# Kernel tuning notes

Hardware: AMD Instinct MI355X
Metric: run time of the kernel (lower is better)

Reference implementation:

```python
import jax, jax.numpy as jnp
import numpy as np

N_NODES = 100000
N_EDGES = 1600000
IN_DIM = 128
N_HID = 128


def setup_inputs() -> dict:
    key = jax.random.key(0)
    k1, k2, k3, k4 = jax.random.split(key, 4)
    node_feature = jax.random.normal(k1, (N_NODES, IN_DIM), dtype=jnp.float32)
    edge_index = jax.random.randint(k2, (2, N_EDGES), 0, N_NODES, dtype=jnp.int64)
    # GCN layer weights (glorot-ish scale)
    W1 = jax.random.normal(k3, (IN_DIM, N_HID), dtype=jnp.float32) / np.sqrt(IN_DIM)
    b1 = jnp.zeros((N_HID,), dtype=jnp.float32)
    W2 = jax.random.normal(k4, (N_HID, N_HID), dtype=jnp.float32) / np.sqrt(N_HID)
    b2 = jnp.zeros((N_HID,), dtype=jnp.float32)
    return {"node_feature": node_feature, "edge_index": edge_index,
            "W1": W1, "b1": b1, "W2": W2, "b2": b2}


def _gcn_layer(x, W, b, row, col, n_nodes):
    """GCNConv: x' = D^-1/2 (A + I) D^-1/2 (x W) + b, symmetric norm with self-loops."""
    xt = x @ W  # [N, out]
    ones = jnp.ones(row.shape[0], dtype=xt.dtype)
    deg = jnp.zeros((n_nodes,), dtype=xt.dtype).at[col].add(ones) + 1.0  # +1 self-loop
    dinv = jax.lax.rsqrt(deg)  # [N]
    norm = dinv[row] * dinv[col]  # [E]
    # gather messages from source (row), scatter-add into destination (col)
    agg = jnp.zeros_like(xt).at[col].add(xt[row] * norm[:, None])
    agg = agg + xt * (dinv * dinv)[:, None]  # self-loop contribution
    return agg + b


def reference(node_feature, edge_index, W1, b1, W2, b2):
    row, col = edge_index[0], edge_index[1]
    n = node_feature.shape[0]
    h = _gcn_layer(node_feature, W1, b1, row, col, n)
    # F.dropout with training=False is identity (eval-mode reference)
    h = _gcn_layer(h, W2, b2, row, col, n)
    return h
```

## Files before the change

### kernel.cpp

```cpp
#include <hip/hip_runtime.h>

typedef unsigned short ushort_t;
typedef __attribute__((ext_vector_type(8))) short short8;
typedef __attribute__((ext_vector_type(8))) unsigned short us8v;
typedef __attribute__((ext_vector_type(4))) float f32x4;

__device__ __forceinline__ float b2f(unsigned short u) {
    union { unsigned int i; float f; } v; v.i = ((unsigned int)u) << 16; return v.f;
}
__device__ __forceinline__ unsigned short f2b(float f) {
    union { float f; unsigned int i; } v; v.f = f;
    unsigned int r = (v.i + 0x7FFF + ((v.i >> 16) & 1)) >> 16;
    return (unsigned short)r;
}

__device__ __forceinline__ void load_edge(const int* __restrict__ ei, int e, int E,
                                          int is64, int& s, int& d) {
    if (is64) {
        const long long* el = (const long long*)ei;
        s = (int)el[e]; d = (int)el[E + e];
    } else {
        s = ei[e]; d = ei[E + e];
    }
}

__device__ __forceinline__ int detect64(const int* __restrict__ ei, int t) {
    int z = 0;
    for (int i = t; i < 512; i += 256) z |= ei[2 * i + 1];
    return (__syncthreads_or(z) == 0);
}

__global__ void k_hist(const int* __restrict__ ei, int E, unsigned N,
                       int* __restrict__ bhist, int BSH, int NB) {
    __shared__ int lh[256];
    int t = threadIdx.x;
    for (int b = t; b < NB; b += 256) lh[b] = 0;
    int is64 = detect64(ei, t);
    int e0 = blockIdx.x * 4096;
    #pragma unroll
    for (int i = 0; i < 16; ++i) {
        int e = e0 + i * 256 + t;
        if (e < E) {
            int s, d; load_edge(ei, e, E, is64, s, d);
            if ((unsigned)s < N && (unsigned)d < N) atomicAdd(&lh[d >> BSH], 1);
        }
    }
    __syncthreads();
    for (int b = t; b < NB; b += 256) { int v = lh[b]; if (v) atomicAdd(&bhist[b], v); }
}

__global__ void k_scanb(const int* __restrict__ bhist, int NB,
                        int* __restrict__ bkbase, int* __restrict__ bkcur) {
    __shared__ int sd[256];
    int t = threadIdx.x;
    int v0 = (t < NB) ? bhist[t] : 0;
    sd[t] = v0;
    for (int o = 1; o < 256; o <<= 1) {
        __syncthreads();
        int v = (t >= o) ? sd[t - o] : 0;
        __syncthreads();
        sd[t] += v;
    }
    __syncthreads();
    if (t < NB) { int ex = sd[t] - v0; bkbase[t] = ex; bkcur[t] = ex; }
}

__global__ __launch_bounds__(256) void k_bucket(const int* __restrict__ ei, int E, unsigned N,
                                                int* __restrict__ bkcur,
                                                int* __restrict__ bs, int* __restrict__ bd,
                                                int BSH, int NB) {
    __shared__ int lss[4096];
    __shared__ int ldd[4096];
    __shared__ int lhist[256];
    __shared__ int lcur[256];
    int t = threadIdx.x;
    int e0 = blockIdx.x * 4096;
    for (int b = t; b < NB; b += 256) lhist[b] = 0;
    int is64 = detect64(ei, t);
    #pragma unroll
    for (int i = 0; i < 16; ++i) {
        int idx = i * 256 + t, e = e0 + idx;
        int s = -1, d = -1;
        if (e < E) {
            load_edge(ei, e, E, is64, s, d);
            if (!((unsigned)s < N && (unsigned)d < N)) d = -1;
        }
        lss[idx] = s; ldd[idx] = d;
        if (d >= 0) atomicAdd(&lhist[d >> BSH], 1);
    }
    __syncthreads();
    for (int b = t; b < NB; b += 256) {
        int v = lhist[b];
        lcur[b] = v ? atomicAdd(&bkcur[b], v) : 0;
    }
    __syncthreads();
    #pragma unroll
    for (int i = 0; i < 16; ++i) {
        int idx = i * 256 + t;
        int d = ldd[idx];
        if (d >= 0) {
            int p = atomicAdd(&lcur[d >> BSH], 1);
            bs[p] = lss[idx]; bd[p] = d;
        }
    }
}

__global__ void k_count2(const int* __restrict__ bd, const int* __restrict__ bkbase,
                         const int* __restrict__ bkcur, int N, int BSH,
                         int* __restrict__ cnt) {
    __shared__ int lc[512];
    int b = blockIdx.x, t = threadIdx.x;
    int nbase = b << BSH;
    int nn = min(1 << BSH, N - nbase);
    for (int j = t; j < nn; j += 256) lc[j] = 0;
    __syncthreads();
    int s0 = bkbase[b], s1 = bkcur[b];
    for (int i = s0 + t; i < s1; i += 256) atomicAdd(&lc[bd[i] - nbase], 1);
    __syncthreads();
    for (int j = t; j < nn; j += 256) cnt[nbase + j] = lc[j];
}

__global__ void k_assign(int* __restrict__ cnt, int N,
                         int* __restrict__ pos, float* __restrict__ dinv,
                         int* __restrict__ cursor, int* __restrict__ srcs,
                         int padidx) {
    __shared__ int sd[256];
    __shared__ int sbase;
    int t = threadIdx.x;
    int n = blockIdx.x * 256 + t;
    int c = (n < N) ? cnt[n] : 0;
    int cp = (c + 7) & ~7;
    sd[t] = cp;
    for (int o = 1; o < 256; o <<= 1) {
        __syncthreads();
        int v = (t >= o) ? sd[t - o] : 0;
        __syncthreads();
        sd[t] += v;
    }
    __syncthreads();
    if (t == 255) sbase = atomicAdd(cursor, sd[255]);
    __syncthreads();
    if (n < N) {
        int st = sbase + sd[t] - cp;
        pos[n] = st;
        dinv[n] = rsqrtf((float)c + 1.0f);
        cnt[n] = cp;
        for (int q = c; q < cp; ++q) srcs[st + q] = padidx;
    }
}

__global__ void k_fill2(const int* __restrict__ bs, const int* __restrict__ bd,
                        const int* __restrict__ bkbase, const int* __restrict__ bkcur,
                        const int* __restrict__ pos, int N, int BSH,
                        int* __restrict__ srcs) {
    __shared__ int lcur[512];
    int b = blockIdx.x, t = threadIdx.x;
    int nbase = b << BSH;
    int nn = min(1 << BSH, N - nbase);
    for (int j = t; j < nn; j += 256) lcur[j] = pos[nbase + j];
    __syncthreads();
    int s0 = bkbase[b], s1 = bkcur[b];
    for (int i = s0 + t; i < s1; i += 256) {
        int d = bd[i];
        int p = atomicAdd(&lcur[d - nbase], 1);
        srcs[p] = bs[i];
    }
}

__global__ void k_transpose(const float* __restrict__ W1, const float* __restrict__ W2,
                            ushort_t* __restrict__ WT, ushort_t* __restrict__ xt,
                            int N) {
    if (blockIdx.x == 2) {
        int t = threadIdx.x;
        if (t < 128) xt[((size_t)N << 7) + t] = 0;
        return;
    }
    const float* src = blockIdx.x ? W2 : W1;
    ushort_t* dst = WT + blockIdx.x * 16384;
    for (int i = threadIdx.x; i < 16384; i += 256) {
        int n = i >> 7, k = i & 127;
        dst[i] = f2b(src[k * 128 + n]);
    }
}

template <bool ABF>
__global__ __launch_bounds__(256) void k_gemm(const void* __restrict__ Ap,
                                              const ushort_t* __restrict__ WT,
                                              ushort_t* __restrict__ C,
                                              const float* __restrict__ dinv, int M) {
    __shared__ __align__(16) ushort_t sA[64 * 136];
    __shared__ __align__(16) ushort_t sW[128 * 136];
    int t = threadIdx.x;
    int row0 = blockIdx.x * 64;

    #pragma unroll
    for (int it = 0; it < 8; ++it) {
        int flat = (it * 256 + t) * 8;
        int n = flat >> 7, k = flat & 127;
        uint4 v = *(const uint4*)(WT + flat);
        *(uint4*)(&sW[n * 136 + k]) = v;
    }
    #pragma unroll
    for (int it = 0; it < 4; ++it) {
        int flat = (it * 256 + t) * 8;
        int r = flat >> 7, cc = flat & 127;
        int row = row0 + r; if (row > M - 1) row = M - 1;
        if (ABF) {
            const ushort_t* A = (const ushort_t*)Ap;
            us8v v = *(const us8v*)(A + ((size_t)row << 7) + cc);
            *(us8v*)(&sA[r * 136 + cc]) = v;
        } else {
            const float* A = (const float*)Ap;
            const float* p = A + (size_t)row * 128 + cc;
            float4 f0 = *(const float4*)p;
            float4 f1 = *(const float4*)(p + 4);
            ushort_t tmp[8] __attribute__((aligned(16)));
            tmp[0] = f2b(f0.x); tmp[1] = f2b(f0.y); tmp[2] = f2b(f0.z); tmp[3] = f2b(f0.w);
            tmp[4] = f2b(f1.x); tmp[5] = f2b(f1.y); tmp[6] = f2b(f1.z); tmp[7] = f2b(f1.w);
            *(uint4*)(&sA[r * 136 + cc]) = *(const uint4*)tmp;
        }
    }
    __syncthreads();

    int w = t >> 6, lane = t & 63;
    int m = lane & 15, quad = lane >> 4;

    f32x4 acc[8] = {};
    #pragma unroll
    for (int k0 = 0; k0 < 128; k0 += 32) {
        short8 af = *(const short8*)(&sA[(w * 16 + m) * 136 + k0 + quad * 8]);
        #pragma unroll
        for (int tt = 0; tt < 8; ++tt) {
            short8 bf = *(const short8*)(&sW[(tt * 16 + m) * 136 + k0 + quad * 8]);
            acc[tt] = __builtin_amdgcn_mfma_f32_16x16x32_bf16(af, bf, acc[tt], 0, 0, 0);
        }
    }
    #pragma unroll
    for (int r = 0; r < 4; ++r) {
        int row = row0 + w * 16 + quad * 4 + r;
        if (row < M) {
            float dd = dinv[row];
            #pragma unroll
            for (int tt = 0; tt < 8; ++tt)
                C[(size_t)row * 128 + tt * 16 + m] = f2b(dd * acc[tt][r]);
        }
    }
}

template <bool OBF>
__global__ __launch_bounds__(256) void k_agg(const ushort_t* __restrict__ xt,
                                             const float* __restrict__ bias,
                                             void* __restrict__ outp,
                                             const int* __restrict__ pos,
                                             const int* __restrict__ cnts,
                                             const float* __restrict__ dinv,
                                             const int* __restrict__ srcs, int N) {
    int lane = threadIdx.x & 63;
    int slot = lane >> 4, j = lane & 15;
    int d = (blockIdx.x << 2) + (threadIdx.x >> 6);
    if (d >= N) return;
    int cn = cnts[d];
    int start = pos[d];
    float dd = dinv[d];
    us8v vs = *(const us8v*)(xt + ((size_t)d << 7) + (j << 3));
    float4 bb0 = *(const float4*)(bias + (j << 3));
    float4 bb1 = *(const float4*)(bias + (j << 3) + 4);

    float a0 = 0.f, a1 = 0.f, a2 = 0.f, a3 = 0.f;
    float a4 = 0.f, a5 = 0.f, a6 = 0.f, a7 = 0.f;

    for (int base = 0; base < cn; base += 64) {
        int n = cn - base; if (n > 64) n = 64;
        int sv = 0;
        if (lane < n) sv = srcs[start + base + lane];
        int s0 = __shfl(sv, slot);
        int s1 = __shfl(sv, 4 + slot);
        us8v v0 = *(const us8v*)(xt + ((size_t)s0 << 7) + (j << 3));
        us8v v1 = *(const us8v*)(xt + ((size_t)s1 << 7) + (j << 3));
        for (int c = 8; c < n; c += 8) {
            int t0 = __shfl(sv, c + slot);
            int t1 = __shfl(sv, c + 4 + slot);
            us8v w0 = *(const us8v*)(xt + ((size_t)t0 << 7) + (j << 3));
            us8v w1 = *(const us8v*)(xt + ((size_t)t1 << 7) + (j << 3));
            a0 += b2f(v0[0]); a1 += b2f(v0[1]); a2 += b2f(v0[2]); a3 += b2f(v0[3]);
            a4 += b2f(v0[4]); a5 += b2f(v0[5]); a6 += b2f(v0[6]); a7 += b2f(v0[7]);
            a0 += b2f(v1[0]); a1 += b2f(v1[1]); a2 += b2f(v1[2]); a3 += b2f(v1[3]);
            a4 += b2f(v1[4]); a5 += b2f(v1[5]); a6 += b2f(v1[6]); a7 += b2f(v1[7]);
            v0 = w0; v1 = w1;
        }
        a0 += b2f(v0[0]); a1 += b2f(v0[1]); a2 += b2f(v0[2]); a3 += b2f(v0[3]);
        a4 += b2f(v0[4]); a5 += b2f(v0[5]); a6 += b2f(v0[6]); a7 += b2f(v0[7]);
        a0 += b2f(v1[0]); a1 += b2f(v1[1]); a2 += b2f(v1[2]); a3 += b2f(v1[3]);
        a4 += b2f(v1[4]); a5 += b2f(v1[5]); a6 += b2f(v1[6]); a7 += b2f(v1[7]);
    }
    a0 += __shfl_xor(a0, 32); a1 += __shfl_xor(a1, 32);
    a2 += __shfl_xor(a2, 32); a3 += __shfl_xor(a3, 32);
    a4 += __shfl_xor(a4, 32); a5 += __shfl_xor(a5, 32);
    a6 += __shfl_xor(a6, 32); a7 += __shfl_xor(a7, 32);
    a0 += __shfl_xor(a0, 16); a1 += __shfl_xor(a1, 16);
    a2 += __shfl_xor(a2, 16); a3 += __shfl_xor(a3, 16);
    a4 += __shfl_xor(a4, 16); a5 += __shfl_xor(a5, 16);
    a6 += __shfl_xor(a6, 16); a7 += __shfl_xor(a7, 16);

    if (slot == 0) {
        float o0 = dd * (a0 + b2f(vs[0])) + bb0.x;
        float o1 = dd * (a1 + b2f(vs[1])) + bb0.y;
        float o2 = dd * (a2 + b2f(vs[2])) + bb0.z;
        float o3 = dd * (a3 + b2f(vs[3])) + bb0.w;
        float o4 = dd * (a4 + b2f(vs[4])) + bb1.x;
        float o5 = dd * (a5 + b2f(vs[5])) + bb1.y;
        float o6 = dd * (a6 + b2f(vs[6])) + bb1.z;
        float o7 = dd * (a7 + b2f(vs[7])) + bb1.w;
        if (OBF) {
            ushort_t tmp[8] __attribute__((aligned(16)));
            tmp[0] = f2b(o0); tmp[1] = f2b(o1); tmp[2] = f2b(o2); tmp[3] = f2b(o3);
            tmp[4] = f2b(o4); tmp[5] = f2b(o5); tmp[6] = f2b(o6); tmp[7] = f2b(o7);
            *(us8v*)((ushort_t*)outp + ((size_t)d << 7) + (j << 3)) = *(const us8v*)tmp;
        } else {
            float4 q0 = { o0, o1, o2, o3 };
            float4 q1 = { o4, o5, o6, o7 };
            float4* po = (float4*)((float*)outp + ((size_t)d << 7) + (j << 3));
            po[0] = q0; po[1] = q1;
        }
    }
}


extern "C" void kernel_launch(void* const* d_in, const int* in_sizes, int n_in,
                              void* d_out, int out_size, void* d_ws, size_t ws_size,
                              hipStream_t stream) {
    const float* x  = (const float*)d_in[0];
    const int*   ei = (const int*)d_in[1];
    const float* W1 = (const float*)d_in[2];
    const float* b1 = (const float*)d_in[3];
    const float* W2 = (const float*)d_in[4];
    const float* b2 = (const float*)d_in[5];
    float* out = (float*)d_out;

    const int N = in_sizes[0] / 128;
    const int E = in_sizes[1] / 2;

    int BSH = 9;
    int NB = (N + (1 << BSH) - 1) >> BSH;
    while (NB > 256) { BSH++; NB = (N + (1 << BSH) - 1) >> BSH; }

    char* ws = (char*)d_ws;
    size_t o = 0;
    auto take = [&](size_t bytes) { size_t r = o; o = (o + bytes + 255) & ~(size_t)255; return r; };
    size_t o_bhist  = take(256 * 4);
    size_t o_cursor = take(4);
    size_t zero_end = o;
    size_t o_bkbase = take(256 * 4);
    size_t o_bkcur  = take(256 * 4);
    size_t o_cnt    = take((size_t)N * 4);
    size_t o_pos    = take((size_t)N * 4);
    size_t o_dinv   = take((size_t)N * 4);
    size_t o_srcs   = take(((size_t)E + 7 * (size_t)N + 64) * 4);
    size_t o_WT     = take(2 * 128 * 128 * 2);
    size_t big_sz   = (size_t)E * 8 > (size_t)(N + 1) * 256 ? (size_t)E * 8
                                                            : (size_t)(N + 1) * 256;
    size_t o_big    = take(big_sz);
    (void)ws_size;

    int*      bhist  = (int*)(ws + o_bhist);
    int*      cursor = (int*)(ws + o_cursor);
    int*      bkbase = (int*)(ws + o_bkbase);
    int*      bkcur  = (int*)(ws + o_bkcur);
    int*      cnt    = (int*)(ws + o_cnt);
    int*      pos    = (int*)(ws + o_pos);
    float*    dinv   = (float*)(ws + o_dinv);
    int*      srcs   = (int*)(ws + o_srcs);
    ushort_t* WT     = (ushort_t*)(ws + o_WT);
    int*      bs     = (int*)(ws + o_big);
    int*      bd     = (int*)(ws + o_big) + E;
    ushort_t* xt     = (ushort_t*)(ws + o_big);
    ushort_t* hbf    = (ushort_t*)d_out;

    hipMemsetAsync(d_ws, 0, zero_end, stream);

    int gE = (E + 4095) / 4096;
    int gN = (N + 255) / 256;
    int gG = (N + 63) / 64;
    int gA = (N + 3) / 4;

    k_hist<<<gE, 256, 0, stream>>>(ei, E, (unsigned)N, bhist, BSH, NB);
    k_scanb<<<1, 256, 0, stream>>>(bhist, NB, bkbase, bkcur);
    k_bucket<<<gE, 256, 0, stream>>>(ei, E, (unsigned)N, bkcur, bs, bd, BSH, NB);
    k_count2<<<NB, 256, 0, stream>>>(bd, bkbase, bkcur, N, BSH, cnt);
    k_assign<<<gN, 256, 0, stream>>>(cnt, N, pos, dinv, cursor, srcs, N);
    k_fill2<<<NB, 256, 0, stream>>>(bs, bd, bkbase, bkcur, pos, N, BSH, srcs);
    k_transpose<<<3, 256, 0, stream>>>(W1, W2, WT, xt, N);

    k_gemm<false><<<gG, 256, 0, stream>>>(x, WT, xt, dinv, N);
    k_agg<true><<<gA, 256, 0, stream>>>(xt, b1, hbf, pos, cnt, dinv, srcs, N);
    k_gemm<true><<<gG, 256, 0, stream>>>(hbf, WT + 16384, xt, dinv, N);
    k_agg<false><<<gA, 256, 0, stream>>>(xt, b2, out, pos, cnt, dinv, srcs, N);
}
```

Before: 345.6 us.

## Fuse CSR construction kernels into one cooperative kernel with grid syncs

Merges the seven preprocessing kernels (histogram, bucket scan, bucketing, count, assign, fill, weight transpose) into a single cooperative launch that separates phases with grid.sync(). The aim is to remove per-launch overhead and idle gaps between the small kernels. If the cooperative launch fails, it falls back to the original multi-kernel path. Cooperative launch needs the whole grid (about 400 blocks using 34KB of LDS each) to be resident at once. Each grid sync also makes every block wait for the slowest one.

Result: slower. 571.5 us (+65.4%).

```diff
diff --git a/kernel.cpp b/kernel.cpp
--- a/kernel.cpp
+++ b/kernel.cpp
@@ -1,4 +1,7 @@
 #include <hip/hip_runtime.h>
+#include <hip/hip_cooperative_groups.h>
+
+namespace cg = cooperative_groups;
 
 typedef unsigned short ushort_t;
 typedef __attribute__((ext_vector_type(8))) short short8;
@@ -28,6 +31,155 @@
     int z = 0;
     for (int i = t; i < 512; i += 256) z |= ei[2 * i + 1];
     return (__syncthreads_or(z) == 0);
+}
+
+__global__ __launch_bounds__(256) void k_csr(
+        const int* __restrict__ ei, int E, unsigned N, int Ni, int NB, int BSH,
+        int nch, int gN,
+        int* __restrict__ bhist, int* __restrict__ bkbase, int* __restrict__ bkcur,
+        int* __restrict__ cnt, int* __restrict__ pos, float* __restrict__ dinv,
+        int* __restrict__ cursor, int* __restrict__ srcs,
+        int* __restrict__ bs, int* __restrict__ bd,
+        const float* __restrict__ W1, const float* __restrict__ W2,
+        ushort_t* __restrict__ WT, ushort_t* __restrict__ xt) {
+    cg::grid_group grid = cg::this_grid();
+    __shared__ int smem[8704];
+    int* lss = smem;
+    int* ldd = smem + 4096;
+    int* lhist = smem + 8192;
+    int* lcur = smem + 8448;
+    int t = threadIdx.x;
+    int b = blockIdx.x;
+
+    if (b < nch) {
+        for (int q = t; q < NB; q += 256) lhist[q] = 0;
+        int is64 = detect64(ei, t);
+        int e0 = b * 4096;
+        #pragma unroll
+        for (int i = 0; i < 16; ++i) {
+            int e = e0 + i * 256 + t;
+            if (e < E) {
+                int s, d; load_edge(ei, e, E, is64, s, d);
+                if ((unsigned)s < N && (unsigned)d < N) atomicAdd(&lhist[d >> BSH], 1);
+            }
+        }
+        __syncthreads();
+        for (int q = t; q < NB; q += 256) {
+            int v = lhist[q]; if (v) atomicAdd(&bhist[q], v);
+        }
+    }
+    grid.sync();
+
+    if (b == 0) {
+        int v0 = (t < NB) ? bhist[t] : 0;
+        smem[t] = v0;
+        for (int o = 1; o < 256; o <<= 1) {
+            __syncthreads();
+            int v = (t >= o) ? smem[t - o] : 0;
+            __syncthreads();
+            smem[t] += v;
+        }
+        __syncthreads();
+        if (t < NB) { int ex = smem[t] - v0; bkbase[t] = ex; bkcur[t] = ex; }
+    }
+    grid.sync();
+
+    if (b < nch) {
+        for (int q = t; q < NB; q += 256) lhist[q] = 0;
+        int is64 = detect64(ei, t);
+        int e0 = b * 4096;
+        #pragma unroll
+        for (int i = 0; i < 16; ++i) {
+            int idx = i * 256 + t, e = e0 + idx;
+            int s = -1, d = -1;
+            if (e < E) {
+                load_edge(ei, e, E, is64, s, d);
+                if (!((unsigned)s < N && (unsigned)d < N)) d = -1;
+            }
+            lss[idx] = s; ldd[idx] = d;
+            if (d >= 0) atomicAdd(&lhist[d >> BSH], 1);
+        }
+        __syncthreads();
+        for (int q = t; q < NB; q += 256) {
+            int v = lhist[q];
+            lcur[q] = v ? atomicAdd(&bkcur[q], v) : 0;
+        }
+        __syncthreads();
+        #pragma unroll
+        for (int i = 0; i < 16; ++i) {
+            int idx = i * 256 + t;
+            int d = ldd[idx];
+            if (d >= 0) {
+                int p = atomicAdd(&lcur[d >> BSH], 1);
+                bs[p] = lss[idx]; bd[p] = d;
+            }
+        }
+    }
+    grid.sync();
+
+    if (b < NB) {
+        int nbase = b << BSH;
+        int nn = min(1 << BSH, Ni - nbase);
+        for (int q = t; q < nn; q += 256) smem[q] = 0;
+        __syncthreads();
+        int s0 = bkbase[b], s1 = bkcur[b];
+        for (int i = s0 + t; i < s1; i += 256) atomicAdd(&smem[bd[i] - nbase], 1);
+        __syncthreads();
+        for (int q = t; q < nn; q += 256) cnt[nbase + q] = smem[q];
+    }
+    grid.sync();
+
+    if (b < gN) {
+        int n = b * 256 + t;
+        int c = (n < Ni) ? cnt[n] : 0;
+        int cp = (c + 7) & ~7;
+        smem[t] = cp;
+        for (int o = 1; o < 256; o <<= 1) {
+            __syncthreads();
+            int v = (t >= o) ? smem[t - o] : 0;
+            __syncthreads();
+            smem[t] += v;
+        }
+        __syncthreads();
+        if (t == 255) smem[256] = atomicAdd(cursor, smem[255]);
+        __syncthreads();
+        int sbase = smem[256];
+        if (n < Ni) {
+            int st = sbase + smem[t] - cp;
+            pos[n] = st;
+            dinv[n] = rsqrtf((float)c + 1.0f);
+            cnt[n] = cp;
+            for (int q = c; q < cp; ++q) srcs[st + q] = Ni;
+        }
+    }
+    grid.sync();
+
+    if (b < NB) {
+        int nbase = b << BSH;
+        int nn = min(1 << BSH, Ni - nbase);
+        for (int q = t; q < nn; q += 256) smem[q] = pos[nbase + q];
+        __syncthreads();
+        int s0 = bkbase[b], s1 = bkcur[b];
+        for (int i = s0 + t; i < s1; i += 256) {
+            int d = bd[i];
+            int p = atomicAdd(&smem[d - nbase], 1);
+            srcs[p] = bs[i];
+        }
+    }
+
+    if (b == nch) {
+        for (int i = t; i < 16384; i += 256) {
+            int n = i >> 7, k = i & 127;
+            WT[i] = f2b(W1[k * 128 + n]);
+        }
+    } else if (b == nch + 1) {
+        for (int i = t; i < 16384; i += 256) {
+            int n = i >> 7, k = i & 127;
+            WT[16384 + i] = f2b(W2[k * 128 + n]);
+        }
+    } else if (b == nch + 2) {
+        if (t < 128) xt[((size_t)Ni << 7) + t] = 0;
+    }
 }
 
 __global__ void k_hist(const int* __restrict__ ei, int E, unsigned N,
@@ -378,18 +530,34 @@
 
     hipMemsetAsync(d_ws, 0, zero_end, stream);
 
-    int gE = (E + 4095) / 4096;
-    int gN = (N + 255) / 256;
-    int gG = (N + 63) / 64;
-    int gA = (N + 3) / 4;
-
-    k_hist<<<gE, 256, 0, stream>>>(ei, E, (unsigned)N, bhist, BSH, NB);
-    k_scanb<<<1, 256, 0, stream>>>(bhist, NB, bkbase, bkcur);
-    k_bucket<<<gE, 256, 0, stream>>>(ei, E, (unsigned)N, bkcur, bs, bd, BSH, NB);
-    k_count2<<<NB, 256, 0, stream>>>(bd, bkbase, bkcur, N, BSH, cnt);
-    k_assign<<<gN, 256, 0, stream>>>(cnt, N, pos, dinv, cursor, srcs, N);
-    k_fill2<<<NB, 256, 0, stream>>>(bs, bd, bkbase, bkcur, pos, N, BSH, srcs);
-    k_transpose<<<3, 256, 0, stream>>>(W1, W2, WT, xt, N);
+    int nch = (E + 4095) / 4096;
+    int gN  = (N + 255) / 256;
+    int gG  = (N + 63) / 64;
+    int gA  = (N + 3) / 4;
+    unsigned Nu = (unsigned)N;
+    int Ni = N;
+
+    int gridc = nch + 3;
+    if (gN > gridc) gridc = gN;
+    if (NB > gridc) gridc = NB;
+
+    void* args[] = { (void*)&ei, (void*)&E, (void*)&Nu, (void*)&Ni, (void*)&NB,
+                     (void*)&BSH, (void*)&nch, (void*)&gN,
+                     (void*)&bhist, (void*)&bkbase, (void*)&bkcur, (void*)&cnt,
+                     (void*)&pos, (void*)&dinv, (void*)&cursor, (void*)&srcs,
+                     (void*)&bs, (void*)&bd, (void*)&W1, (void*)&W2,
+                     (void*)&WT, (void*)&xt };
+    hipError_t rc = hipLaunchCooperativeKernel((const void*)k_csr, dim3(gridc),
+                                               dim3(256), args, 0, stream);
+    if (rc != hipSuccess) {
+        k_hist<<<nch, 256, 0, stream>>>(ei, E, Nu, bhist, BSH, NB);
+        k_scanb<<<1, 256, 0, stream>>>(bhist, NB, bkbase, bkcur);
+        k_bucket<<<nch, 256, 0, stream>>>(ei, E, Nu, bkcur, bs, bd, BSH, NB);
+        k_count2<<<NB, 256, 0, stream>>>(bd, bkbase, bkcur, N, BSH, cnt);
+        k_assign<<<gN, 256, 0, stream>>>(cnt, N, pos, dinv, cursor, srcs, N);
+        k_fill2<<<NB, 256, 0, stream>>>(bs, bd, bkbase, bkcur, pos, N, BSH, srcs);
+        k_transpose<<<3, 256, 0, stream>>>(W1, W2, WT, xt, N);
+    }
 
     k_gemm<false><<<gG, 256, 0, stream>>>(x, WT, xt, dinv, N);
     k_agg<true><<<gA, 256, 0, stream>>>(xt, b1, hbf, pos, cnt, dinv, srcs, N);
```

## Fuse CSR count/assign/fill into one per-bucket kernel and fold transposes

Applied to the files above, without the earlier changes.

Merges the per-bucket count, global padded scan and fill kernels into a single per-bucket kernel that counts, scans within the bucket and scatters sources. Each bucket now gets a deterministic segment base (bucket base plus worst-case padding), so the global atomic cursor goes away. The weight transpose moves into spare blocks of the histogram kernel, and the zero pad row is written by the first GEMM. This cuts four launches and the round trips of cnt/pos through global memory. In exchange, srcs is over-allocated for padding and the CSR layout has gaps between buckets.

Result: faster. 330.7 us (-4.3%).

```diff
diff --git a/kernel.cpp b/kernel.cpp
--- a/kernel.cpp
+++ b/kernel.cpp
@@ -30,13 +30,27 @@
     return (__syncthreads_or(z) == 0);
 }
 
-__global__ void k_hist(const int* __restrict__ ei, int E, unsigned N,
-                       int* __restrict__ bhist, int BSH, int NB) {
+__global__ __launch_bounds__(256) void k_histT(const int* __restrict__ ei, int E,
+                                               unsigned N, int* __restrict__ bhist,
+                                               int BSH, int NB, int nch,
+                                               const float* __restrict__ W1,
+                                               const float* __restrict__ W2,
+                                               ushort_t* __restrict__ WT) {
     __shared__ int lh[256];
     int t = threadIdx.x;
-    for (int b = t; b < NB; b += 256) lh[b] = 0;
+    int b = blockIdx.x;
+    if (b >= nch) {
+        const float* src = (b == nch) ? W1 : W2;
+        ushort_t* dst = WT + (b - nch) * 16384;
+        for (int i = t; i < 16384; i += 256) {
+            int n = i >> 7, k = i & 127;
+            dst[i] = f2b(src[k * 128 + n]);
+        }
+        return;
+    }
+    for (int q = t; q < NB; q += 256) lh[q] = 0;
     int is64 = detect64(ei, t);
-    int e0 = blockIdx.x * 4096;
+    int e0 = b * 4096;
     #pragma unroll
     for (int i = 0; i < 16; ++i) {
         int e = e0 + i * 256 + t;
@@ -46,7 +60,7 @@
         }
     }
     __syncthreads();
-    for (int b = t; b < NB; b += 256) { int v = lh[b]; if (v) atomicAdd(&bhist[b], v); }
+    for (int q = t; q < NB; q += 256) { int v = lh[q]; if (v) atomicAdd(&bhist[q], v); }
 }
 
 __global__ void k_scanb(const int* __restrict__ bhist, int NB,
@@ -105,85 +119,66 @@
     }
 }
 
-__global__ void k_count2(const int* __restrict__ bd, const int* __restrict__ bkbase,
-                         const int* __restrict__ bkcur, int N, int BSH,
-                         int* __restrict__ cnt) {
+__global__ __launch_bounds__(256) void k_caf(const int* __restrict__ bs,
+                                             const int* __restrict__ bd,
+                                             const int* __restrict__ bkbase,
+                                             const int* __restrict__ bkcur,
+                                             int N, int BSH,
+                                             int* __restrict__ pos,
+                                             int* __restrict__ cnt,
+                                             float* __restrict__ dinv,
+                                             int* __restrict__ srcs) {
     __shared__ int lc[512];
+    __shared__ int sc[512];
     int b = blockIdx.x, t = threadIdx.x;
     int nbase = b << BSH;
     int nn = min(1 << BSH, N - nbase);
-    for (int j = t; j < nn; j += 256) lc[j] = 0;
+    int segbase = bkbase[b] + b * (7 << BSH);
+
+    lc[t] = 0; lc[t + 256] = 0;
     __syncthreads();
     int s0 = bkbase[b], s1 = bkcur[b];
     for (int i = s0 + t; i < s1; i += 256) atomicAdd(&lc[bd[i] - nbase], 1);
     __syncthreads();
-    for (int j = t; j < nn; j += 256) cnt[nbase + j] = lc[j];
-}
-
-__global__ void k_assign(int* __restrict__ cnt, int N,
-                         int* __restrict__ pos, float* __restrict__ dinv,
-                         int* __restrict__ cursor, int* __restrict__ srcs,
-                         int padidx) {
-    __shared__ int sd[256];
-    __shared__ int sbase;
-    int t = threadIdx.x;
-    int n = blockIdx.x * 256 + t;
-    int c = (n < N) ? cnt[n] : 0;
-    int cp = (c + 7) & ~7;
-    sd[t] = cp;
-    for (int o = 1; o < 256; o <<= 1) {
+
+    int c0 = (t < nn) ? lc[t] : 0;
+    int c1 = (t + 256 < nn) ? lc[t + 256] : 0;
+    int p0 = (c0 + 7) & ~7;
+    int p1 = (c1 + 7) & ~7;
+    sc[t] = p0; sc[t + 256] = p1;
+    __syncthreads();
+    for (int o = 1; o < 512; o <<= 1) {
+        int v0 = (t >= o) ? sc[t - o] : 0;
+        int v1 = (t + 256 >= o) ? sc[t + 256 - o] : 0;
         __syncthreads();
-        int v = (t >= o) ? sd[t - o] : 0;
+        sc[t] += v0; sc[t + 256] += v1;
         __syncthreads();
-        sd[t] += v;
-    }
-    __syncthreads();
-    if (t == 255) sbase = atomicAdd(cursor, sd[255]);
-    __syncthreads();
-    if (n < N) {
-        int st = sbase + sd[t] - cp;
-        pos[n] = st;
-        dinv[n] = rsqrtf((float)c + 1.0f);
-        cnt[n] = cp;
-        for (int q = c; q < cp; ++q) srcs[st + q] = padidx;
-    }
-}
-
-__global__ void k_fill2(const int* __restrict__ bs, const int* __restrict__ bd,
-                        const int* __restrict__ bkbase, const int* __restrict__ bkcur,
-                        const int* __restrict__ pos, int N, int BSH,
-                        int* __restrict__ srcs) {
-    __shared__ int lcur[512];
-    int b = blockIdx.x, t = threadIdx.x;
-    int nbase = b << BSH;
-    int nn = min(1 << BSH, N - nbase);
-    for (int j = t; j < nn; j += 256) lcur[j] = pos[nbase + j];
-    __syncthreads();
-    int s0 = bkbase[b], s1 = bkcur[b];
+    }
+    if (t < nn) {
+        int st = segbase + sc[t] - p0;
+        pos[nbase + t] = st;
+        cnt[nbase + t] = p0;
+        dinv[nbase + t] = rsqrtf((float)c0 + 1.0f);
+        for (int q = c0; q < p0; ++q) srcs[st + q] = N;
+        lc[t] = st;
+    }
+    if (t + 256 < nn) {
+        int st = segbase + sc[t + 256] - p1;
+        pos[nbase + t + 256] = st;
+        cnt[nbase + t + 256] = p1;
+        dinv[nbase + t + 256] = rsqrtf((float)c1 + 1.0f);
+        for (int q = c1; q < p1; ++q) srcs[st + q] = N;
+        lc[t + 256] = st;
+    }
+    __syncthreads();
     for (int i = s0 + t; i < s1; i += 256) {
         int d = bd[i];
-        int p = atomicAdd(&lcur[d - nbase], 1);
+        int p = atomicAdd(&lc[d - nbase], 1);
         srcs[p] = bs[i];
     }
 }
 
-__global__ void k_transpose(const float* __restrict__ W1, const float* __restrict__ W2,
-                            ushort_t* __restrict__ WT, ushort_t* __restrict__ xt,
-                            int N) {
-    if (blockIdx.x == 2) {
-        int t = threadIdx.x;
-        if (t < 128) xt[((size_t)N << 7) + t] = 0;
-        return;
-    }
-    const float* src = blockIdx.x ? W2 : W1;
-    ushort_t* dst = WT + blockIdx.x * 16384;
-    for (int i = threadIdx.x; i < 16384; i += 256) {
-        int n = i >> 7, k = i & 127;
-        dst[i] = f2b(src[k * 128 + n]);
-    }
-}
-
-template <bool ABF>
+template <bool ABF, bool ZROW>
 __global__ __launch_bounds__(256) void k_gemm(const void* __restrict__ Ap,
                                               const ushort_t* __restrict__ WT,
                                               ushort_t* __restrict__ C,
@@ -192,6 +187,8 @@
     __shared__ __align__(16) ushort_t sW[128 * 136];
     int t = threadIdx.x;
     int row0 = blockIdx.x * 64;
+
+    if (ZROW && blockIdx.x == 0 && t < 128) C[((size_t)M << 7) + t] = 0;
 
     #pragma unroll
     for (int it = 0; it < 8; ++it) {
@@ -348,14 +345,13 @@
     size_t o = 0;
     auto take = [&](size_t bytes) { size_t r = o; o = (o + bytes + 255) & ~(size_t)255; return r; };
     size_t o_bhist  = take(256 * 4);
-    size_t o_cursor = take(4);
     size_t zero_end = o;
     size_t o_bkbase = take(256 * 4);
     size_t o_bkcur  = take(256 * 4);
     size_t o_cnt    = take((size_t)N * 4);
     size_t o_pos    = take((size_t)N * 4);
     size_t o_dinv   = take((size_t)N * 4);
-    size_t o_srcs   = take(((size_t)E + 7 * (size_t)N + 64) * 4);
+    size_t o_srcs   = take(((size_t)E + (size_t)NB * (7 << BSH) + 64) * 4);
     size_t o_WT     = take(2 * 128 * 128 * 2);
     size_t big_sz   = (size_t)E * 8 > (size_t)(N + 1) * 256 ? (size_t)E * 8
                                                             : (size_t)(N + 1) * 256;
@@ -363,7 +359,6 @@
     (void)ws_size;
 
     int*      bhist  = (int*)(ws + o_bhist);
-    int*      cursor = (int*)(ws + o_cursor);
     int*      bkbase = (int*)(ws + o_bkbase);
     int*      bkcur  = (int*)(ws + o_bkcur);
     int*      cnt    = (int*)(ws + o_cnt);
@@ -378,21 +373,18 @@
 
     hipMemsetAsync(d_ws, 0, zero_end, stream);
 
-    int gE = (E + 4095) / 4096;
-    int gN = (N + 255) / 256;
-    int gG = (N + 63) / 64;
-    int gA = (N + 3) / 4;
-
-    k_hist<<<gE, 256, 0, stream>>>(ei, E, (unsigned)N, bhist, BSH, NB);
+    int nch = (E + 4095) / 4096;
+    int gG  = (N + 63) / 64;
+    int gA  = (N + 3) / 4;
+    unsigned Nu = (unsigned)N;
+
+    k_histT<<<nch + 2, 256, 0, stream>>>(ei, E, Nu, bhist, BSH, NB, nch, W1, W2, WT);
     k_scanb<<<1, 256, 0, stream>>>(bhist, NB, bkbase, bkcur);
-    k_bucket<<<gE, 256, 0, stream>>>(ei, E, (unsigned)N, bkcur, bs, bd, BSH, NB);
-    k_count2<<<NB, 256, 0, stream>>>(bd, bkbase, bkcur, N, BSH, cnt);
-    k_assign<<<gN, 256, 0, stream>>>(cnt, N, pos, dinv, cursor, srcs, N);
-    k_fill2<<<NB, 256, 0, stream>>>(bs, bd, bkbase, bkcur, pos, N, BSH, srcs);
-    k_transpose<<<3, 256, 0, stream>>>(W1, W2, WT, xt, N);
-
-    k_gemm<false><<<gG, 256, 0, stream>>>(x, WT, xt, dinv, N);
+    k_bucket<<<nch, 256, 0, stream>>>(ei, E, Nu, bkcur, bs, bd, BSH, NB);
+    k_caf<<<NB, 256, 0, stream>>>(bs, bd, bkbase, bkcur, N, BSH, pos, cnt, dinv, srcs);
+
+    k_gemm<false, true><<<gG, 256, 0, stream>>>(x, WT, xt, dinv, N);
     k_agg<true><<<gA, 256, 0, stream>>>(xt, b1, hbf, pos, cnt, dinv, srcs, N);
-    k_gemm<true><<<gG, 256, 0, stream>>>(hbf, WT + 16384, xt, dinv, N);
+    k_gemm<true, false><<<gG, 256, 0, stream>>>(hbf, WT + 16384, xt, dinv, N);
     k_agg<false><<<gA, 256, 0, stream>>>(xt, b2, out, pos, cnt, dinv, srcs, N);
 }
```
